# Kernel tuning notes

Hardware: AMD Instinct MI355X
Metric: run time of the kernel (lower is better)

## Reference

```python
import jax, jax.numpy as jnp
import numpy as np

B, H_IMG, W_IMG = 8, 64, 64
C, HEADS, SR, MSG = 128, 4, 4, 4
N0 = H_IMG * W_IMG


def _linear(x, w, b):
    return x @ w.T + b


def _layernorm(x, g, b, eps=1e-5):
    mu = jnp.mean(x, -1, keepdims=True)
    var = jnp.mean(jnp.square(x - mu), -1, keepdims=True)
    return (x - mu) * jax.lax.rsqrt(var + eps) * g + b


def _conv2d(x, w, b, stride, pad, groups=1):
    y = jax.lax.conv_general_dilated(
        x, w, (stride, stride), [(pad, pad), (pad, pad)],
        dimension_numbers=("NCHW", "OIHW", "NCHW"), feature_group_count=groups)
    return y + b[None, :, None, None]


def setup_inputs():
    key = jax.random.key(0)
    ks = jax.random.split(key, 16)
    def nrm(k, shape, std=0.02):
        return jax.random.normal(k, shape, jnp.float32) * std
    z = lambda *s: jnp.zeros(s, jnp.float32)
    return {
        "x": jax.random.normal(ks[0], (B, N0, C), jnp.float32),
        "msg_tokens": jax.random.normal(ks[1], (B, MSG, C), jnp.float32),
        "Wq": nrm(ks[2], (C, C)), "bq": z(C),
        "sr1_w": nrm(ks[3], (C, C, 4, 4), float(np.sqrt(2.0 / (16 * C)))), "sr1_b": z(C),
        "ln1_g": jnp.ones((C,), jnp.float32), "ln1_b": z(C),
        "sr2_w": nrm(ks[4], (C, C, 2, 2), float(np.sqrt(2.0 / (4 * C)))), "sr2_b": z(C),
        "ln2_g": jnp.ones((C,), jnp.float32), "ln2_b": z(C),
        "kv1_w": nrm(ks[5], (C, C)), "kv1_b": z(C),
        "kv2_w": nrm(ks[6], (C, C)), "kv2_b": z(C),
        "lc1_w": nrm(ks[7], (C // 2, 1, 3, 3), float(np.sqrt(2.0 / 9.0))), "lc1_b": z(C // 2),
        "lc2_w": nrm(ks[8], (C // 2, 1, 3, 3), float(np.sqrt(2.0 / 9.0))), "lc2_b": z(C // 2),
        "proj_w": nrm(ks[9], (C, C)), "proj_b": z(C),
        "H": H_IMG, "W": W_IMG,
    }


def reference(x, msg_tokens, Wq, bq, sr1_w, sr1_b, ln1_g, ln1_b,
              sr2_w, sr2_b, ln2_g, ln2_b, kv1_w, kv1_b, kv2_w, kv2_b,
              lc1_w, lc1_b, lc2_w, lc2_b, proj_w, proj_b, H, W):
    Bsz, _, Cc = x.shape
    m = msg_tokens.shape[1]
    h = HEADS
    dh = Cc // h
    scale = dh ** -0.5
    x_q = jnp.concatenate([x, msg_tokens], axis=1)       # [B, N, C]
    N = x_q.shape[1]
    q = _linear(x_q, Wq, bq).reshape(Bsz, N, h, dh).transpose(0, 2, 1, 3)  # [B,h,N,dh]
    x_img = x.transpose(0, 2, 1).reshape(Bsz, Cc, H, W)

    def branch(sr_w, sr_b, ln_g, ln_b, kv_w, kv_b, lc_w, lc_b, q_half, stride):
        Hr, Wr = H // stride, W // stride
        L = Hr * Wr
        # spatial reduction conv -> tokens
        xr = _conv2d(x_img, sr_w, sr_b, stride, 0).reshape(Bsz, Cc, L).transpose(0, 2, 1)
        # message tokens pass through the SR conv via summed weights
        msg_r = jnp.einsum('bnc,oc->bno', msg_tokens, sr_w.sum((-1, -2))) + sr_b
        xk = jax.nn.gelu(_layernorm(jnp.concatenate([xr, msg_r], 1), ln_g, ln_b), approximate=False)
        kv = _linear(xk, kv_w, kv_b).reshape(Bsz, L + m, 2, h // 2, dh).transpose(2, 0, 3, 1, 4)
        k, v = kv[0], kv[1]                               # [B, h/2, L+m, dh]
        attn = jax.nn.softmax(jnp.einsum('bhnd,bhld->bhnl', q_half, k) * scale, axis=-1)
        # fused depthwise conv on the spatial part of V (message tokens bypass)
        v_flat = v.transpose(0, 2, 1, 3).reshape(Bsz, L + m, Cc // 2).transpose(0, 2, 1)  # [B,C/2,L+m]
        lc = _conv2d(v_flat[:, :, :L].reshape(Bsz, Cc // 2, Hr, Wr), lc_w, lc_b, 1, 1,
                     groups=Cc // 2).reshape(Bsz, Cc // 2, L)
        v_add = jnp.concatenate([lc, v_flat[:, :, L:]], axis=2)
        v = v + v_add.reshape(Bsz, h // 2, dh, L + m).transpose(0, 1, 3, 2)
        return jnp.einsum('bhnl,bhld->bhnd', attn, v).transpose(0, 2, 1, 3).reshape(Bsz, N, Cc // 2)

    x1 = branch(sr1_w, sr1_b, ln1_g, ln1_b, kv1_w, kv1_b, lc1_w, lc1_b, q[:, :h // 2], SR)
    x2 = branch(sr2_w, sr2_b, ln2_g, ln2_b, kv2_w, kv2_b, lc2_w, lc2_b, q[:, h // 2:], SR // 2)
    out = _linear(jnp.concatenate([x1, x2], -1), proj_w, proj_b)
    out = x_q + out                                       # identity = x_q, drop_path = Identity
    return out[:, :-m], out[:, -m:]
```

## Files before the change

kernel.cpp:

```cpp
#include <hip/hip_runtime.h>
#include <math.h>

#define BB 8
#define CC 128
#define N0 4096
#define MSGN 4
#define NTOT 4100
#define IMG 64
#define NPAD 4224
#define LMP1 320
#define LMP2 1088

#define OFF_WFQ    0
#define OFF_WFKV1  8192
#define OFF_WFKV2  16384
#define OFF_WFPROJ 24576
#define OFF_WFSR1  32768
#define OFF_WFSR2  163840
#define OFF_QH     196608
#define OFF_XK1    2359296
#define OFF_XK2    2492416
#define OFF_KV1O   3018752
#define OFF_KV2O   3284992
#define OFF_KH1    4337664
#define OFF_VT1    4419584
#define OFF_KH2    4501504
#define OFF_VT2    4780032
#define OFF_XP     5058560

typedef _Float16 half8v __attribute__((ext_vector_type(8)));
typedef _Float16 half4v __attribute__((ext_vector_type(4)));
typedef float f32x4 __attribute__((ext_vector_type(4)));

__device__ __forceinline__ size_t af_idx(int m, int k, int Kc) {
    return ((size_t)((m >> 4) * Kc + (k >> 5)) * 64 + ((k >> 3) & 3) * 16 + (m & 15)) * 8 + (k & 7);
}

__device__ __forceinline__ float exp2_fast(float x) {
#if __has_builtin(__builtin_amdgcn_exp2f)
    return __builtin_amdgcn_exp2f(x);
#else
    return __expf(x * 0.6931471805599453f);
#endif
}

__device__ __forceinline__ void gload16(const _Float16* g, _Float16* l) {
    __builtin_amdgcn_global_load_lds(
        (const __attribute__((address_space(1))) unsigned int*)g,
        (__attribute__((address_space(3))) unsigned int*)l, 16, 0, 0);
}

__global__ void prep_weights(const float* __restrict__ Wq, const float* __restrict__ kv1,
                             const float* __restrict__ kv2, const float* __restrict__ proj,
                             const float* __restrict__ sr1w, const float* __restrict__ sr2w,
                             float* __restrict__ ws, _Float16* __restrict__ Qh) {
    int u = blockIdx.x * blockDim.x + threadIdx.x;
    if (u >= 49152) {
        int idx = u - 49152;
        if (idx >= BB * 4 * (NPAD - NTOT) * 32) return;
        int d = idx & 31;
        int rest = idx >> 5;
        int n = NTOT + rest % (NPAD - NTOT);
        int rest2 = rest / (NPAD - NTOT);
        int hg = rest2 & 3;
        int b = rest2 >> 2;
        Qh[((size_t)(b * 4 + hg) * NPAD + n) * 32 + d] = (_Float16)0.f;
        return;
    }
    int seg, base;
    const float* w = nullptr;
    _Float16* dst;
    if (u < 2048)        { seg = 0; base = u;          w = Wq;   dst = (_Float16*)(ws + OFF_WFQ); }
    else if (u < 4096)   { seg = 0; base = u - 2048;   w = kv1;  dst = (_Float16*)(ws + OFF_WFKV1); }
    else if (u < 6144)   { seg = 0; base = u - 4096;   w = kv2;  dst = (_Float16*)(ws + OFF_WFKV2); }
    else if (u < 8192)   { seg = 0; base = u - 6144;   w = proj; dst = (_Float16*)(ws + OFF_WFPROJ); }
    else if (u < 40960)  { seg = 1; base = u - 8192;   w = sr1w; dst = (_Float16*)(ws + OFF_WFSR1); }
    else                 { seg = 2; base = u - 40960;  w = sr2w; dst = (_Float16*)(ws + OFF_WFSR2); }
    int lane = base & 63;
    int t = (base >> 6) & 7;
    int kc = base >> 9;
    int n = t * 16 + (lane & 15);
    int k0 = kc * 32 + (lane >> 4) * 8;
    half8v val;
    #pragma unroll
    for (int j = 0; j < 8; ++j) {
        int k = k0 + j;
        float v;
        if (seg == 0) v = w[n * 128 + k];
        else if (seg == 1) v = w[(n * 128 + (k & 127)) * 16 + (k >> 7)];
        else v = w[(n * 128 + (k & 127)) * 4 + (k >> 7)];
        val[j] = (_Float16)v;
    }
    *(half8v*)(dst + (size_t)base * 8) = val;
}

template<int S, int WR, int LL, int LM, int KW>
__device__ __forceinline__ void sr_partial(
    int mtile, int kcbase, int lane, const float* __restrict__ x,
    const float* __restrict__ msg, const _Float16* __restrict__ Wf, f32x4 acc[8]) {
    int m15 = lane & 15, quadk = lane >> 4;
    int m = mtile * 16 + m15;
    bool valid = m < BB * LM;
    const float* base = x;
    bool isimg = false;
    if (valid) {
        int b = m / LM, tok = m - b * LM;
        if (tok < LL) {
            int hr = tok / WR, wr = tok - hr * WR;
            base = x + ((size_t)b * N0 + hr * S * IMG + wr * S) * 128;
            isimg = true;
        } else {
            base = msg + ((size_t)b * MSGN + (tok - LL)) * 128;
        }
    }
    const half8v* Bp = (const half8v*)Wf + lane;
    for (int kk = 0; kk < KW; ++kk) {
        int kc = kcbase + kk;
        int k0 = (kc * 4 + quadk) * 8;
        int c = k0 & 127, ij = k0 >> 7;
        half8v a;
        if (valid) {
            int off;
            if (isimg) {
                int ki = ij / S, kj = ij - ki * S;
                off = (ki * IMG + kj) * 128 + c;
            } else off = c;
            const float4* p4 = (const float4*)(base + off);
            float4 f0 = p4[0], f1 = p4[1];
            a[0] = (_Float16)f0.x; a[1] = (_Float16)f0.y; a[2] = (_Float16)f0.z; a[3] = (_Float16)f0.w;
            a[4] = (_Float16)f1.x; a[5] = (_Float16)f1.y; a[6] = (_Float16)f1.z; a[7] = (_Float16)f1.w;
        } else {
            #pragma unroll
            for (int j = 0; j < 8; ++j) a[j] = (_Float16)0.f;
        }
        #pragma unroll
        for (int t = 0; t < 8; ++t)
            acc[t] = __builtin_amdgcn_mfma_f32_16x16x32_f16(a, Bp[(size_t)(kc * 8 + t) * 64], acc[t], 0, 0, 0);
    }
}

__global__ __launch_bounds__(256) void input_gemms(
    const float* __restrict__ x, const float* __restrict__ msg,
    const _Float16* __restrict__ Wf1, const _Float16* __restrict__ Wf2,
    const float* __restrict__ b1, const float* __restrict__ g1, const float* __restrict__ be1,
    const float* __restrict__ b2, const float* __restrict__ g2, const float* __restrict__ be2,
    _Float16* __restrict__ XK1, _Float16* __restrict__ XK2,
    const _Float16* __restrict__ WfQ, const float* __restrict__ bq,
    _Float16* __restrict__ Qh) {
    __shared__ float red[4][2048];
    int tid = threadIdx.x;
    int lane = tid & 63, wave = tid >> 6;
    int bid = blockIdx.x;

    if (bid >= 261) {
        int u = (bid - 261) * 4 + wave;
        int mt = u >> 1, nh = u & 1;
        int m15 = lane & 15, quadk = lane >> 4;
        int m = mt * 16 + m15;
        bool valid = m < BB * NTOT;
        const float* rowp = x;
        if (valid) {
            int b = m / NTOT, n = m - b * NTOT;
            rowp = (n < N0) ? (x + ((size_t)b * N0 + n) * 128)
                            : (msg + ((size_t)b * MSGN + (n - N0)) * 128);
        }
        const half8v* Bp = (const half8v*)WfQ + lane;
        f32x4 acc[4];
        #pragma unroll
        for (int t = 0; t < 4; ++t) acc[t] = (f32x4){0.f, 0.f, 0.f, 0.f};
        #pragma unroll
        for (int kc = 0; kc < 4; ++kc) {
            half8v a;
            if (valid) {
                const float4* p4 = (const float4*)(rowp + (kc * 4 + quadk) * 8);
                float4 f0 = p4[0], f1 = p4[1];
                a[0] = (_Float16)f0.x; a[1] = (_Float16)f0.y; a[2] = (_Float16)f0.z; a[3] = (_Float16)f0.w;
                a[4] = (_Float16)f1.x; a[5] = (_Float16)f1.y; a[6] = (_Float16)f1.z; a[7] = (_Float16)f1.w;
            } else {
                #pragma unroll
                for (int j = 0; j < 8; ++j) a[j] = (_Float16)0.f;
            }
            #pragma unroll
            for (int t = 0; t < 4; ++t)
                acc[t] = __builtin_amdgcn_mfma_f32_16x16x32_f16(a, Bp[(size_t)(kc * 8 + nh * 4 + t) * 64], acc[t], 0, 0, 0);
        }
        int quad = lane >> 4, n15 = lane & 15;
        const float qscale = 0.17677669529663687f * 1.4426950408889634f;
        #pragma unroll
        for (int r = 0; r < 4; ++r) {
            int mm = mt * 16 + quad * 4 + r;
            if (mm >= BB * NTOT) continue;
            int b = mm / NTOT, tok = mm - b * NTOT;
            #pragma unroll
            for (int t = 0; t < 4; ++t) {
                int n = nh * 64 + t * 16 + n15;
                Qh[((size_t)(b * 4 + (n >> 5)) * NPAD + tok) * 32 + (n & 31)] =
                    (_Float16)((acc[t][r] + bq[n]) * qscale);
            }
        }
        return;
    }

    if (bid >= 132) {
        int mtile = (bid - 132) * 4 + wave;
        f32x4 acc[8];
        #pragma unroll
        for (int t = 0; t < 8; ++t) acc[t] = (f32x4){0.f, 0.f, 0.f, 0.f};
        sr_partial<2, 32, 1024, 1028, 16>(mtile, 0, lane, x, msg, Wf2, acc);
        int quad = lane >> 4, n15 = lane & 15;
        float bb[8], gg[8], eb[8];
        #pragma unroll
        for (int j = 0; j < 8; ++j) {
            bb[j] = b2[j * 16 + n15];
            gg[j] = g2[j * 16 + n15];
            eb[j] = be2[j * 16 + n15];
        }
        #pragma unroll
        for (int r = 0; r < 4; ++r) {
            int m = mtile * 16 + quad * 4 + r;
            float s = 0.f;
            #pragma unroll
            for (int j = 0; j < 8; ++j) s += acc[j][r] + bb[j];
            #pragma unroll
            for (int off = 1; off < 16; off <<= 1) s += __shfl_xor(s, off);
            float mu = s * (1.f / 128.f);
            float q = 0.f;
            #pragma unroll
            for (int j = 0; j < 8; ++j) { float d = acc[j][r] + bb[j] - mu; q += d * d; }
            #pragma unroll
            for (int off = 1; off < 16; off <<= 1) q += __shfl_xor(q, off);
            float rs = rsqrtf(q * (1.f / 128.f) + 1e-5f);
            if (m < 8224) {
                #pragma unroll
                for (int j = 0; j < 8; ++j) {
                    float y = (acc[j][r] + bb[j] - mu) * rs * gg[j] + eb[j];
                    y = 0.5f * y * (1.f + erff(y * 0.70710678118654752f));
                    XK2[af_idx(m, j * 16 + n15, 4)] = (_Float16)y;
                }
            }
        }
        return;
    }

    f32x4 acc[8];
    #pragma unroll
    for (int t = 0; t < 8; ++t) acc[t] = (f32x4){0.f, 0.f, 0.f, 0.f};
    int mtile = bid;
    sr_partial<4, 16, 256, 260, 16>(mtile, wave * 16, lane, x, msg, Wf1, acc);
    int quad = lane >> 4, n15 = lane & 15;
    #pragma unroll
    for (int t = 0; t < 8; ++t)
        #pragma unroll
        for (int r = 0; r < 4; ++r)
            red[wave][(quad * 4 + r) * 128 + t * 16 + n15] = acc[t][r];
    __syncthreads();
    for (int e = tid; e < 2048; e += 256)
        red[0][e] = red[0][e] + red[1][e] + red[2][e] + red[3][e];
    __syncthreads();
    int r16 = tid >> 4, l16 = tid & 15;
    int m = mtile * 16 + r16;
    float v[8];
    float s = 0.f;
    #pragma unroll
    for (int j = 0; j < 8; ++j) { v[j] = red[0][r16 * 128 + j * 16 + l16] + b1[j * 16 + l16]; s += v[j]; }
    #pragma unroll
    for (int off = 1; off < 16; off <<= 1) s += __shfl_xor(s, off);
    float mu = s * (1.f / 128.f);
    float q = 0.f;
    #pragma unroll
    for (int j = 0; j < 8; ++j) { v[j] -= mu; q += v[j] * v[j]; }
    #pragma unroll
    for (int off = 1; off < 16; off <<= 1) q += __shfl_xor(q, off);
    float rs = rsqrtf(q * (1.f / 128.f) + 1e-5f);
    if (m < 2080) {
        #pragma unroll
        for (int j = 0; j < 8; ++j) {
            int n = j * 16 + l16;
            float y = v[j] * rs * g1[n] + be1[n];
            y = 0.5f * y * (1.f + erff(y * 0.70710678118654752f));
            XK1[af_idx(m, n, 4)] = (_Float16)y;
        }
    }
}

__global__ __launch_bounds__(256) void kv_gemm(
    const _Float16* __restrict__ XK1, const _Float16* __restrict__ XK2,
    const _Float16* __restrict__ Wf1, const _Float16* __restrict__ Wf2,
    const float* __restrict__ b1, const float* __restrict__ b2,
    float* __restrict__ o1, float* __restrict__ o2) {
    int lane = threadIdx.x & 63, wave = threadIdx.x >> 6;
    int u = blockIdx.x * 4 + wave;
    int t = u >> 1, nh = u & 1;
    int lt;
    const half8v* Ap;
    const half8v* Bp;
    const float* bias;
    float* outp;
    if (t < 130) { lt = t;       Ap = (const half8v*)XK1 + (size_t)lt * 4 * 64 + lane; Bp = (const half8v*)Wf1 + lane; bias = b1; outp = o1; }
    else         { lt = t - 130; Ap = (const half8v*)XK2 + (size_t)lt * 4 * 64 + lane; Bp = (const half8v*)Wf2 + lane; bias = b2; outp = o2; }
    f32x4 acc[4];
    #pragma unroll
    for (int tt = 0; tt < 4; ++tt) acc[tt] = (f32x4){0.f, 0.f, 0.f, 0.f};
    #pragma unroll
    for (int kc = 0; kc < 4; ++kc) {
        half8v a = Ap[(size_t)kc * 64];
        #pragma unroll
        for (int tt = 0; tt < 4; ++tt)
            acc[tt] = __builtin_amdgcn_mfma_f32_16x16x32_f16(a, Bp[(size_t)(kc * 8 + nh * 4 + tt) * 64], acc[tt], 0, 0, 0);
    }
    int quad = lane >> 4, n15 = lane & 15;
    #pragma unroll
    for (int r = 0; r < 4; ++r) {
        int m = lt * 16 + quad * 4 + r;
        #pragma unroll
        for (int tt = 0; tt < 4; ++tt) {
            int n = nh * 64 + tt * 16 + n15;
            outp[(size_t)m * 128 + n] = acc[tt][r] + bias[n];
        }
    }
}

__global__ void pack_kv(const float* __restrict__ kv1o, const float* __restrict__ kv2o,
                        const float* __restrict__ lc1w, const float* __restrict__ lc1b,
                        const float* __restrict__ lc2w, const float* __restrict__ lc2b,
                        _Float16* __restrict__ Kh1, _Float16* __restrict__ Vt1,
                        _Float16* __restrict__ Kh2, _Float16* __restrict__ Vt2) {
    int idx = blockIdx.x * 256 + threadIdx.x;
    const int T1 = BB * LMP1 * 64;
    const float* kv;
    const float* lcw;
    const float* lcb;
    _Float16* Kh;
    _Float16* Vt;
    int Wr, L, Lm, Lmp, li;
    if (idx < T1) { li = idx;      kv = kv1o; lcw = lc1w; lcb = lc1b; Kh = Kh1; Vt = Vt1; Wr = 16; L = 256;  Lm = 260;  Lmp = LMP1; }
    else          { li = idx - T1; kv = kv2o; lcw = lc2w; lcb = lc2b; Kh = Kh2; Vt = Vt2; Wr = 32; L = 1024; Lm = 1028; Lmp = LMP2; }
    int ch = li & 63;
    int rest = li >> 6;
    int n = rest % Lmp;
    int b = rest / Lmp;
    int h2 = ch >> 5, d = ch & 31;
    int Hr = L / Wr;
    float kval = 0.f, vnew = 0.f;
    if (n < Lm) {
        const float* kvb = kv + (size_t)b * Lm * 128;
        kval = kvb[(size_t)n * 128 + ch];
        float v = kvb[(size_t)n * 128 + 64 + ch];
        float add;
        if (n < L) {
            int hr = n / Wr, wr = n - hr * Wr;
            float sum = lcb[ch];
            #pragma unroll
            for (int ki = 0; ki < 3; ++ki)
                #pragma unroll
                for (int kj = 0; kj < 3; ++kj) {
                    int y = hr + ki - 1, xx = wr + kj - 1;
                    if ((unsigned)y < (unsigned)Hr && (unsigned)xx < (unsigned)Wr)
                        sum += lcw[ch * 9 + ki * 3 + kj] * kvb[((size_t)y * Wr + xx) * 128 + 64 + ch];
                }
            add = sum;
        } else {
            add = v;
        }
        vnew = v + add;
    }
    Kh[((size_t)(b * 2 + h2) * Lmp + n) * 32 + d] = (_Float16)kval;
    Vt[(size_t)(b * 2 + h2) * Lmp * 32 + (size_t)(n >> 2) * 128
       + (d & 15) * 8 + ((d >> 4) << 2) + (n & 3)] = (_Float16)vnew;
}

__global__ __launch_bounds__(256, 4) void attn_mfma(
    const _Float16* __restrict__ Qh,
    const _Float16* __restrict__ Kh1, const _Float16* __restrict__ Vt1,
    const _Float16* __restrict__ Kh2, const _Float16* __restrict__ Vt2,
    _Float16* __restrict__ XP) {
    __shared__ _Float16 sK[2][2048];
    __shared__ _Float16 sV[2][2048];
    int tid = threadIdx.x;
    int lane = tid & 63, wave = tid >> 6;
    int b = blockIdx.y;
    int z = blockIdx.z;
    int h2 = z & 1, br = 1 - (z >> 1);
    int tile = blockIdx.x * 4 + wave;
    int n0 = tile * 32;
    int q16 = lane & 15, quad = lane >> 4;
    const f32x4 zf = {0.f, 0.f, 0.f, 0.f};
    int NT = br ? (LMP2 / 64) : (LMP1 / 64);
    int Lmp = br ? LMP2 : LMP1;
    const _Float16* kb = (br ? Kh2 : Kh1) + (size_t)(b * 2 + h2) * Lmp * 32;
    const _Float16* vb = (br ? Vt2 : Vt1) + (size_t)(b * 2 + h2) * Lmp * 32;
    int hg = br * 2 + h2;
    const _Float16* qp = Qh + ((size_t)(b * 4 + hg) * NPAD + n0 + q16) * 32 + quad * 8;
    half8v qf0 = *(const half8v*)qp;
    half8v qf1 = *(const half8v*)(qp + 512);
    f32x4 O00 = zf, O01 = zf, O10 = zf, O11 = zf;
    float la = 0.f, lb = 0.f;

    int ksrc = (wave * 16 + q16) * 32 + quad * 8;
    int vsrc = wave * 512 + lane * 8;

    gload16(kb + ksrc, &sK[0][wave * 512]);
    gload16(vb + vsrc, &sV[0][wave * 512]);
    __syncthreads();

    for (int t = 0; t < NT; ++t) {
        int cur = t & 1;
        if (t + 1 < NT) {
            size_t o = (size_t)(t + 1) * 2048;
            gload16(kb + o + ksrc, &sK[cur ^ 1][wave * 512]);
            gload16(vb + o + vsrc, &sV[cur ^ 1][wave * 512]);
        }
        half8v kf[4], vv[4];
        #pragma unroll
        for (int i = 0; i < 4; ++i)
            kf[i] = *(const half8v*)&sK[cur][i * 512 + lane * 8];
        #pragma unroll
        for (int i = 0; i < 4; ++i)
            vv[i] = *(const half8v*)&sV[cur][i * 512 + quad * 128 + q16 * 8];

        half4v p0[4], p1[4];
        #pragma unroll
        for (int i = 0; i < 4; ++i) {
            f32x4 s0 = __builtin_amdgcn_mfma_f32_16x16x32_f16(kf[i], qf0, zf, 0, 0, 0);
            f32x4 s1 = __builtin_amdgcn_mfma_f32_16x16x32_f16(kf[i], qf1, zf, 0, 0, 0);
            half4v a, c;
            #pragma unroll
            for (int r = 0; r < 4; ++r) {
                float e0 = exp2_fast(s0[r]); la += e0; a[r] = (_Float16)e0;
                float e1 = exp2_fast(s1[r]); lb += e1; c[r] = (_Float16)e1;
            }
            p0[i] = a; p1[i] = c;
        }
        #pragma unroll
        for (int i = 0; i < 4; ++i) {
            half4v v0 = __builtin_shufflevector(vv[i], vv[i], 0, 1, 2, 3);
            half4v v1 = __builtin_shufflevector(vv[i], vv[i], 4, 5, 6, 7);
            O00 = __builtin_amdgcn_mfma_f32_16x16x16f16(p0[i], v0, O00, 0, 0, 0);
            O01 = __builtin_amdgcn_mfma_f32_16x16x16f16(p0[i], v1, O01, 0, 0, 0);
            O10 = __builtin_amdgcn_mfma_f32_16x16x16f16(p1[i], v0, O10, 0, 0, 0);
            O11 = __builtin_amdgcn_mfma_f32_16x16x16f16(p1[i], v1, O11, 0, 0, 0);
        }
        __syncthreads();
    }

    la += __shfl_xor(la, 16); la += __shfl_xor(la, 32);
    lb += __shfl_xor(lb, 16); lb += __shfl_xor(lb, 32);
    la -= 60.0f; lb -= 60.0f;
    float ia = 1.0f / la;
    float ib = 1.0f / lb;

    int kbase = br * 64 + h2 * 32;
    #pragma unroll
    for (int r = 0; r < 4; ++r) {
        int row = quad * 4 + r;
        int src = (lane & 48) | row;
        float fa = __shfl(ia, src);
        float fb = __shfl(ib, src);
        int n = n0 + row;
        if (n < NTOT) {
            int m = b * NTOT + n;
            XP[af_idx(m, kbase + q16, 4)] = (_Float16)(O00[r] * fa);
            XP[af_idx(m, kbase + 16 + q16, 4)] = (_Float16)(O01[r] * fa);
        }
        int n2 = n + 16;
        if (n2 < NTOT) {
            int m = b * NTOT + n2;
            XP[af_idx(m, kbase + q16, 4)] = (_Float16)(O10[r] * fb);
            XP[af_idx(m, kbase + 16 + q16, 4)] = (_Float16)(O11[r] * fb);
        }
    }
}

__global__ __launch_bounds__(256) void proj_gemm(
    const _Float16* __restrict__ XP,
    const _Float16* __restrict__ Wf, const float* __restrict__ bias,
    float* __restrict__ out_f32, const float* __restrict__ x, const float* __restrict__ msg) {
    int lane = threadIdx.x & 63, wave = threadIdx.x >> 6;
    int u = blockIdx.x * 4 + wave;
    int mt = u >> 1, nh = u & 1;
    const half8v* Ap = (const half8v*)XP + (size_t)mt * 4 * 64 + lane;
    const half8v* Bp = (const half8v*)Wf + lane;
    f32x4 acc[4];
    #pragma unroll
    for (int t = 0; t < 4; ++t) acc[t] = (f32x4){0.f, 0.f, 0.f, 0.f};
    #pragma unroll
    for (int kc = 0; kc < 4; ++kc) {
        half8v a = Ap[(size_t)kc * 64];
        #pragma unroll
        for (int t = 0; t < 4; ++t)
            acc[t] = __builtin_amdgcn_mfma_f32_16x16x32_f16(a, Bp[(size_t)(kc * 8 + nh * 4 + t) * 64], acc[t], 0, 0, 0);
    }
    int quad = lane >> 4, n15 = lane & 15;
    #pragma unroll
    for (int r = 0; r < 4; ++r) {
        int m = mt * 16 + quad * 4 + r;
        if (m >= BB * NTOT) continue;
        int b = m / NTOT, tok = m - b * NTOT;
        const float* rp;
        float* dst;
        if (tok < N0) {
            rp = x + ((size_t)b * N0 + tok) * 128;
            dst = out_f32 + ((size_t)b * N0 + tok) * 128;
        } else {
            rp = msg + ((size_t)b * MSGN + (tok - N0)) * 128;
            dst = out_f32 + (size_t)BB * N0 * 128 + ((size_t)b * MSGN + (tok - N0)) * 128;
        }
        #pragma unroll
        for (int t = 0; t < 4; ++t) {
            int n = nh * 64 + t * 16 + n15;
            dst[n] = acc[t][r] + bias[n] + rp[n];
        }
    }
}

extern "C" void kernel_launch(void* const* d_in, const int* in_sizes, int n_in,
                              void* d_out, int out_size, void* d_ws, size_t ws_size,
                              hipStream_t stream) {
    const float* x     = (const float*)d_in[0];
    const float* msg   = (const float*)d_in[1];
    const float* Wq    = (const float*)d_in[2];
    const float* bq    = (const float*)d_in[3];
    const float* sr1w  = (const float*)d_in[4];
    const float* sr1b  = (const float*)d_in[5];
    const float* ln1g  = (const float*)d_in[6];
    const float* ln1b  = (const float*)d_in[7];
    const float* sr2w  = (const float*)d_in[8];
    const float* sr2b  = (const float*)d_in[9];
    const float* ln2g  = (const float*)d_in[10];
    const float* ln2b  = (const float*)d_in[11];
    const float* kv1w  = (const float*)d_in[12];
    const float* kv1b  = (const float*)d_in[13];
    const float* kv2w  = (const float*)d_in[14];
    const float* kv2b  = (const float*)d_in[15];
    const float* lc1w  = (const float*)d_in[16];
    const float* lc1b  = (const float*)d_in[17];
    const float* lc2w  = (const float*)d_in[18];
    const float* lc2b  = (const float*)d_in[19];
    const float* projw = (const float*)d_in[20];
    const float* projb = (const float*)d_in[21];
    float* ws  = (float*)d_ws;
    float* out = (float*)d_out;

    _Float16* WfQ    = (_Float16*)(ws + OFF_WFQ);
    _Float16* WfKV1  = (_Float16*)(ws + OFF_WFKV1);
    _Float16* WfKV2  = (_Float16*)(ws + OFF_WFKV2);
    _Float16* WfPROJ = (_Float16*)(ws + OFF_WFPROJ);
    _Float16* WfSR1  = (_Float16*)(ws + OFF_WFSR1);
    _Float16* WfSR2  = (_Float16*)(ws + OFF_WFSR2);
    _Float16* Qh     = (_Float16*)(ws + OFF_QH);
    _Float16* XP     = (_Float16*)(ws + OFF_XP);
    _Float16* XK1    = (_Float16*)(ws + OFF_XK1);
    _Float16* XK2    = (_Float16*)(ws + OFF_XK2);
    float* kv1o      = ws + OFF_KV1O;
    float* kv2o      = ws + OFF_KV2O;
    _Float16* Kh1    = (_Float16*)(ws + OFF_KH1);
    _Float16* Vt1    = (_Float16*)(ws + OFF_VT1);
    _Float16* Kh2    = (_Float16*)(ws + OFF_KH2);
    _Float16* Vt2    = (_Float16*)(ws + OFF_VT2);

    prep_weights<<<688, 256, 0, stream>>>(Wq, kv1w, kv2w, projw, sr1w, sr2w, ws, Qh);
    input_gemms<<<1286, 256, 0, stream>>>(x, msg, WfSR1, WfSR2,
                                          sr1b, ln1g, ln1b, sr2b, ln2g, ln2b,
                                          XK1, XK2, WfQ, bq, Qh);
    kv_gemm<<<322, 256, 0, stream>>>(XK1, XK2, WfKV1, WfKV2, kv1b, kv2b, kv1o, kv2o);
    pack_kv<<<2816, 256, 0, stream>>>(kv1o, kv2o, lc1w, lc1b, lc2w, lc2b,
                                      Kh1, Vt1, Kh2, Vt2);
    attn_mfma<<<dim3(33, 8, 4), 256, 0, stream>>>(Qh, Kh1, Vt1, Kh2, Vt2, XP);
    proj_gemm<<<1025, 256, 0, stream>>>(XP, WfPROJ, projb, out, x, msg);
}
```

Baseline: 190.9 us.

## Fuse KV GEMM into input_gemms epilogue and compute softmax denominators via MFMA

The KV projection GEMM now runs inside input_gemms, reading the LayerNorm+GELU output from shared memory instead of a global XK buffer. The K half is written directly in the head-packed fp16 layout and only V goes to a smaller fp32 buffer, which removes the separate kv_gemm launch and halves the data pack_kv reads. K padding rows are now zeroed in prep_weights. In attention, the row sums are accumulated by an extra MFMA against a ones vector instead of scalar adds plus shuffles, which adds matrix work but removes VALU and cross-lane reductions.

```diff
diff --git a/kernel.cpp b/kernel.cpp
--- a/kernel.cpp
+++ b/kernel.cpp
@@ -53,11 +53,27 @@
 __global__ void prep_weights(const float* __restrict__ Wq, const float* __restrict__ kv1,
                              const float* __restrict__ kv2, const float* __restrict__ proj,
                              const float* __restrict__ sr1w, const float* __restrict__ sr2w,
-                             float* __restrict__ ws, _Float16* __restrict__ Qh) {
+                             float* __restrict__ ws, _Float16* __restrict__ Qh,
+                             _Float16* __restrict__ Kh1, _Float16* __restrict__ Kh2) {
     int u = blockIdx.x * blockDim.x + threadIdx.x;
+    if (u >= 176128) {
+        int e = u - 176128;
+        int d = e & 31;
+        int rest = e >> 5;
+        if (rest < 960) {
+            int n = 260 + rest % 60;
+            int bh = rest / 60;
+            Kh1[((size_t)bh * LMP1 + n) * 32 + d] = (_Float16)0.f;
+        } else {
+            rest -= 960;
+            int n = 1028 + rest % 60;
+            int bh = rest / 60;
+            Kh2[((size_t)bh * LMP2 + n) * 32 + d] = (_Float16)0.f;
+        }
+        return;
+    }
     if (u >= 49152) {
         int idx = u - 49152;
-        if (idx >= BB * 4 * (NPAD - NTOT) * 32) return;
         int d = idx & 31;
         int rest = idx >> 5;
         int n = NTOT + rest % (NPAD - NTOT);
@@ -144,13 +160,17 @@
     const _Float16* __restrict__ Wf1, const _Float16* __restrict__ Wf2,
     const float* __restrict__ b1, const float* __restrict__ g1, const float* __restrict__ be1,
     const float* __restrict__ b2, const float* __restrict__ g2, const float* __restrict__ be2,
-    _Float16* __restrict__ XK1, _Float16* __restrict__ XK2,
+    const _Float16* __restrict__ WfKV1, const _Float16* __restrict__ WfKV2,
+    const float* __restrict__ kvb1, const float* __restrict__ kvb2,
+    _Float16* __restrict__ Kh1, float* __restrict__ vo1,
+    _Float16* __restrict__ Kh2, float* __restrict__ vo2,
     const _Float16* __restrict__ WfQ, const float* __restrict__ bq,
     _Float16* __restrict__ Qh) {
     __shared__ float red[4][2048];
     int tid = threadIdx.x;
     int lane = tid & 63, wave = tid >> 6;
     int bid = blockIdx.x;
+    const f32x4 zf4 = {0.f, 0.f, 0.f, 0.f};
 
     if (bid >= 261) {
         int u = (bid - 261) * 4 + wave;
@@ -167,7 +187,7 @@
         const half8v* Bp = (const half8v*)WfQ + lane;
         f32x4 acc[4];
         #pragma unroll
-        for (int t = 0; t < 4; ++t) acc[t] = (f32x4){0.f, 0.f, 0.f, 0.f};
+        for (int t = 0; t < 4; ++t) acc[t] = zf4;
         #pragma unroll
         for (int kc = 0; kc < 4; ++kc) {
             half8v a;
@@ -205,7 +225,7 @@
         int mtile = (bid - 132) * 4 + wave;
         f32x4 acc[8];
         #pragma unroll
-        for (int t = 0; t < 8; ++t) acc[t] = (f32x4){0.f, 0.f, 0.f, 0.f};
+        for (int t = 0; t < 8; ++t) acc[t] = zf4;
         sr_partial<2, 32, 1024, 1028, 16>(mtile, 0, lane, x, msg, Wf2, acc);
         int quad = lane >> 4, n15 = lane & 15;
         float bb[8], gg[8], eb[8];
@@ -215,9 +235,9 @@
             gg[j] = g2[j * 16 + n15];
             eb[j] = be2[j * 16 + n15];
         }
+        _Float16* XKw = (_Float16*)(&red[0][0]) + wave * 2176;
         #pragma unroll
         for (int r = 0; r < 4; ++r) {
-            int m = mtile * 16 + quad * 4 + r;
             float s = 0.f;
             #pragma unroll
             for (int j = 0; j < 8; ++j) s += acc[j][r] + bb[j];
@@ -230,12 +250,38 @@
             #pragma unroll
             for (int off = 1; off < 16; off <<= 1) q += __shfl_xor(q, off);
             float rs = rsqrtf(q * (1.f / 128.f) + 1e-5f);
-            if (m < 8224) {
-                #pragma unroll
-                for (int j = 0; j < 8; ++j) {
-                    float y = (acc[j][r] + bb[j] - mu) * rs * gg[j] + eb[j];
-                    y = 0.5f * y * (1.f + erff(y * 0.70710678118654752f));
-                    XK2[af_idx(m, j * 16 + n15, 4)] = (_Float16)y;
+            #pragma unroll
+            for (int j = 0; j < 8; ++j) {
+                float y = (acc[j][r] + bb[j] - mu) * rs * gg[j] + eb[j];
+                y = 0.5f * y * (1.f + erff(y * 0.70710678118654752f));
+                XKw[(quad * 4 + r) * 136 + j * 16 + n15] = (_Float16)y;
+            }
+        }
+        __syncthreads();
+        const half8v* Bp = (const half8v*)WfKV2 + lane;
+        f32x4 ka[8];
+        #pragma unroll
+        for (int tt = 0; tt < 8; ++tt) ka[tt] = zf4;
+        #pragma unroll
+        for (int kc = 0; kc < 4; ++kc) {
+            half8v a = *(const half8v*)&XKw[(lane & 15) * 136 + kc * 32 + (lane >> 4) * 8];
+            #pragma unroll
+            for (int tt = 0; tt < 8; ++tt)
+                ka[tt] = __builtin_amdgcn_mfma_f32_16x16x32_f16(a, Bp[(size_t)(kc * 8 + tt) * 64], ka[tt], 0, 0, 0);
+        }
+        #pragma unroll
+        for (int r = 0; r < 4; ++r) {
+            int m = mtile * 16 + quad * 4 + r;
+            if (m >= 8224) continue;
+            int b = m / 1028, tok = m - b * 1028;
+            #pragma unroll
+            for (int tt = 0; tt < 8; ++tt) {
+                int n = tt * 16 + n15;
+                float val = ka[tt][r] + kvb2[n];
+                if (tt < 4) {
+                    Kh2[((size_t)(b * 2 + (n >> 5)) * LMP2 + tok) * 32 + (n & 31)] = (_Float16)val;
+                } else {
+                    vo2[((size_t)b * 1028 + tok) * 64 + (n - 64)] = val;
                 }
             }
         }
@@ -244,7 +290,7 @@
 
     f32x4 acc[8];
     #pragma unroll
-    for (int t = 0; t < 8; ++t) acc[t] = (f32x4){0.f, 0.f, 0.f, 0.f};
+    for (int t = 0; t < 8; ++t) acc[t] = zf4;
     int mtile = bid;
     sr_partial<4, 16, 256, 260, 16>(mtile, wave * 16, lane, x, msg, Wf1, acc);
     int quad = lane >> 4, n15 = lane & 15;
@@ -272,80 +318,70 @@
     #pragma unroll
     for (int off = 1; off < 16; off <<= 1) q += __shfl_xor(q, off);
     float rs = rsqrtf(q * (1.f / 128.f) + 1e-5f);
+    _Float16* XKs = (_Float16*)(&red[1][0]);
     if (m < 2080) {
         #pragma unroll
         for (int j = 0; j < 8; ++j) {
-            int n = j * 16 + l16;
-            float y = v[j] * rs * g1[n] + be1[n];
+            float y = v[j] * rs * g1[j * 16 + l16] + be1[j * 16 + l16];
             y = 0.5f * y * (1.f + erff(y * 0.70710678118654752f));
-            XK1[af_idx(m, n, 4)] = (_Float16)y;
-        }
-    }
-}
-
-__global__ __launch_bounds__(256) void kv_gemm(
-    const _Float16* __restrict__ XK1, const _Float16* __restrict__ XK2,
-    const _Float16* __restrict__ Wf1, const _Float16* __restrict__ Wf2,
-    const float* __restrict__ b1, const float* __restrict__ b2,
-    float* __restrict__ o1, float* __restrict__ o2) {
-    int lane = threadIdx.x & 63, wave = threadIdx.x >> 6;
-    int u = blockIdx.x * 4 + wave;
-    int t = u >> 1, nh = u & 1;
-    int lt;
-    const half8v* Ap;
-    const half8v* Bp;
-    const float* bias;
-    float* outp;
-    if (t < 130) { lt = t;       Ap = (const half8v*)XK1 + (size_t)lt * 4 * 64 + lane; Bp = (const half8v*)Wf1 + lane; bias = b1; outp = o1; }
-    else         { lt = t - 130; Ap = (const half8v*)XK2 + (size_t)lt * 4 * 64 + lane; Bp = (const half8v*)Wf2 + lane; bias = b2; outp = o2; }
-    f32x4 acc[4];
-    #pragma unroll
-    for (int tt = 0; tt < 4; ++tt) acc[tt] = (f32x4){0.f, 0.f, 0.f, 0.f};
-    #pragma unroll
-    for (int kc = 0; kc < 4; ++kc) {
-        half8v a = Ap[(size_t)kc * 64];
-        #pragma unroll
-        for (int tt = 0; tt < 4; ++tt)
-            acc[tt] = __builtin_amdgcn_mfma_f32_16x16x32_f16(a, Bp[(size_t)(kc * 8 + nh * 4 + tt) * 64], acc[tt], 0, 0, 0);
-    }
-    int quad = lane >> 4, n15 = lane & 15;
-    #pragma unroll
-    for (int r = 0; r < 4; ++r) {
-        int m = lt * 16 + quad * 4 + r;
-        #pragma unroll
-        for (int tt = 0; tt < 4; ++tt) {
-            int n = nh * 64 + tt * 16 + n15;
-            outp[(size_t)m * 128 + n] = acc[tt][r] + bias[n];
-        }
-    }
-}
-
-__global__ void pack_kv(const float* __restrict__ kv1o, const float* __restrict__ kv2o,
+            XKs[r16 * 136 + j * 16 + l16] = (_Float16)y;
+        }
+    }
+    __syncthreads();
+    {
+        const half8v* Bp = (const half8v*)WfKV1 + lane;
+        int t0 = wave * 2;
+        f32x4 ka[2];
+        ka[0] = zf4; ka[1] = zf4;
+        #pragma unroll
+        for (int kc = 0; kc < 4; ++kc) {
+            half8v a = *(const half8v*)&XKs[(lane & 15) * 136 + kc * 32 + (lane >> 4) * 8];
+            #pragma unroll
+            for (int tt = 0; tt < 2; ++tt)
+                ka[tt] = __builtin_amdgcn_mfma_f32_16x16x32_f16(a, Bp[(size_t)(kc * 8 + t0 + tt) * 64], ka[tt], 0, 0, 0);
+        }
+        #pragma unroll
+        for (int r = 0; r < 4; ++r) {
+            int mm = mtile * 16 + quad * 4 + r;
+            if (mm >= 2080) continue;
+            int b = mm / 260, tok = mm - b * 260;
+            #pragma unroll
+            for (int tt = 0; tt < 2; ++tt) {
+                int n = (t0 + tt) * 16 + n15;
+                float val = ka[tt][r] + kvb1[n];
+                if (n < 64) {
+                    Kh1[((size_t)(b * 2 + (n >> 5)) * LMP1 + tok) * 32 + (n & 31)] = (_Float16)val;
+                } else {
+                    vo1[((size_t)b * 260 + tok) * 64 + (n - 64)] = val;
+                }
+            }
+        }
+    }
+}
+
+__global__ void pack_kv(const float* __restrict__ vo1, const float* __restrict__ vo2,
                         const float* __restrict__ lc1w, const float* __restrict__ lc1b,
                         const float* __restrict__ lc2w, const float* __restrict__ lc2b,
-                        _Float16* __restrict__ Kh1, _Float16* __restrict__ Vt1,
-                        _Float16* __restrict__ Kh2, _Float16* __restrict__ Vt2) {
+                        _Float16* __restrict__ Vt1, _Float16* __restrict__ Vt2) {
     int idx = blockIdx.x * 256 + threadIdx.x;
     const int T1 = BB * LMP1 * 64;
-    const float* kv;
+    const float* vo;
     const float* lcw;
     const float* lcb;
-    _Float16* Kh;
     _Float16* Vt;
     int Wr, L, Lm, Lmp, li;
-    if (idx < T1) { li = idx;      kv = kv1o; lcw = lc1w; lcb = lc1b; Kh = Kh1; Vt = Vt1; Wr = 16; L = 256;  Lm = 260;  Lmp = LMP1; }
-    else          { li = idx - T1; kv = kv2o; lcw = lc2w; lcb = lc2b; Kh = Kh2; Vt = Vt2; Wr = 32; L = 1024; Lm = 1028; Lmp = LMP2; }
+    if (idx < T1) { li = idx;      vo = vo1; lcw = lc1w; lcb = lc1b; Vt = Vt1; Wr = 16; L = 256;  Lm = 260;  Lmp = LMP1; }
+    else          { li = idx - T1; vo = vo2; lcw = lc2w; lcb = lc2b; Vt = Vt2; Wr = 32; L = 1024; Lm = 1028; Lmp = LMP2; }
     int ch = li & 63;
     int rest = li >> 6;
     int n = rest % Lmp;
     int b = rest / Lmp;
     int h2 = ch >> 5, d = ch & 31;
     int Hr = L / Wr;
-    float kval = 0.f, vnew = 0.f;
+    float vnew = 0.f;
     if (n < Lm) {
-        const float* kvb = kv + (size_t)b * Lm * 128;
-        kval = kvb[(size_t)n * 128 + ch];
-        float v = kvb[(size_t)n * 128 + 64 + ch];
+        const float* vb2 = vo + (size_t)b * Lm * 64;
+        float v = vb2[(size_t)n * 64 + ch];
         float add;
         if (n < L) {
             int hr = n / Wr, wr = n - hr * Wr;
@@ -356,7 +392,7 @@
                 for (int kj = 0; kj < 3; ++kj) {
                     int y = hr + ki - 1, xx = wr + kj - 1;
                     if ((unsigned)y < (unsigned)Hr && (unsigned)xx < (unsigned)Wr)
-                        sum += lcw[ch * 9 + ki * 3 + kj] * kvb[((size_t)y * Wr + xx) * 128 + 64 + ch];
+                        sum += lcw[ch * 9 + ki * 3 + kj] * vb2[((size_t)y * Wr + xx) * 64 + ch];
                 }
             add = sum;
         } else {
@@ -364,7 +400,6 @@
         }
         vnew = v + add;
     }
-    Kh[((size_t)(b * 2 + h2) * Lmp + n) * 32 + d] = (_Float16)kval;
     Vt[(size_t)(b * 2 + h2) * Lmp * 32 + (size_t)(n >> 2) * 128
        + (d & 15) * 8 + ((d >> 4) << 2) + (n & 3)] = (_Float16)vnew;
 }
@@ -394,7 +429,10 @@
     half8v qf0 = *(const half8v*)qp;
     half8v qf1 = *(const half8v*)(qp + 512);
     f32x4 O00 = zf, O01 = zf, O10 = zf, O11 = zf;
-    float la = 0.f, lb = 0.f;
+    f32x4 La = zf, Lb = zf;
+    half4v ones4;
+    #pragma unroll
+    for (int r = 0; r < 4; ++r) ones4[r] = (_Float16)1.f;
 
     int ksrc = (wave * 16 + q16) * 32 + quad * 8;
     int vsrc = wave * 512 + lane * 8;
@@ -426,8 +464,8 @@
             half4v a, c;
             #pragma unroll
             for (int r = 0; r < 4; ++r) {
-                float e0 = exp2_fast(s0[r]); la += e0; a[r] = (_Float16)e0;
-                float e1 = exp2_fast(s1[r]); lb += e1; c[r] = (_Float16)e1;
+                a[r] = (_Float16)exp2_fast(s0[r]);
+                c[r] = (_Float16)exp2_fast(s1[r]);
             }
             p0[i] = a; p1[i] = c;
         }
@@ -437,26 +475,20 @@
             half4v v1 = __builtin_shufflevector(vv[i], vv[i], 4, 5, 6, 7);
             O00 = __builtin_amdgcn_mfma_f32_16x16x16f16(p0[i], v0, O00, 0, 0, 0);
             O01 = __builtin_amdgcn_mfma_f32_16x16x16f16(p0[i], v1, O01, 0, 0, 0);
+            La  = __builtin_amdgcn_mfma_f32_16x16x16f16(p0[i], ones4, La, 0, 0, 0);
             O10 = __builtin_amdgcn_mfma_f32_16x16x16f16(p1[i], v0, O10, 0, 0, 0);
             O11 = __builtin_amdgcn_mfma_f32_16x16x16f16(p1[i], v1, O11, 0, 0, 0);
+            Lb  = __builtin_amdgcn_mfma_f32_16x16x16f16(p1[i], ones4, Lb, 0, 0, 0);
         }
         __syncthreads();
     }
 
-    la += __shfl_xor(la, 16); la += __shfl_xor(la, 32);
-    lb += __shfl_xor(lb, 16); lb += __shfl_xor(lb, 32);
-    la -= 60.0f; lb -= 60.0f;
-    float ia = 1.0f / la;
-    float ib = 1.0f / lb;
-
     int kbase = br * 64 + h2 * 32;
     #pragma unroll
     for (int r = 0; r < 4; ++r) {
-        int row = quad * 4 + r;
-        int src = (lane & 48) | row;
-        float fa = __shfl(ia, src);
-        float fb = __shfl(ib, src);
-        int n = n0 + row;
+        float fa = 1.0f / (La[r] - 60.0f);
+        float fb = 1.0f / (Lb[r] - 60.0f);
+        int n = n0 + quad * 4 + r;
         if (n < NTOT) {
             int m = b * NTOT + n;
             XP[af_idx(m, kbase + q16, 4)] = (_Float16)(O00[r] * fa);
@@ -549,22 +581,20 @@
     _Float16* WfSR2  = (_Float16*)(ws + OFF_WFSR2);
     _Float16* Qh     = (_Float16*)(ws + OFF_QH);
     _Float16* XP     = (_Float16*)(ws + OFF_XP);
-    _Float16* XK1    = (_Float16*)(ws + OFF_XK1);
-    _Float16* XK2    = (_Float16*)(ws + OFF_XK2);
-    float* kv1o      = ws + OFF_KV1O;
-    float* kv2o      = ws + OFF_KV2O;
+    float* vo1       = ws + OFF_KV1O;
+    float* vo2       = ws + OFF_KV2O;
     _Float16* Kh1    = (_Float16*)(ws + OFF_KH1);
     _Float16* Vt1    = (_Float16*)(ws + OFF_VT1);
     _Float16* Kh2    = (_Float16*)(ws + OFF_KH2);
     _Float16* Vt2    = (_Float16*)(ws + OFF_VT2);
 
-    prep_weights<<<688, 256, 0, stream>>>(Wq, kv1w, kv2w, projw, sr1w, sr2w, ws, Qh);
+    prep_weights<<<928, 256, 0, stream>>>(Wq, kv1w, kv2w, projw, sr1w, sr2w, ws, Qh, Kh1, Kh2);
     input_gemms<<<1286, 256, 0, stream>>>(x, msg, WfSR1, WfSR2,
                                           sr1b, ln1g, ln1b, sr2b, ln2g, ln2b,
-                                          XK1, XK2, WfQ, bq, Qh);
-    kv_gemm<<<322, 256, 0, stream>>>(XK1, XK2, WfKV1, WfKV2, kv1b, kv2b, kv1o, kv2o);
-    pack_kv<<<2816, 256, 0, stream>>>(kv1o, kv2o, lc1w, lc1b, lc2w, lc2b,
-                                      Kh1, Vt1, Kh2, Vt2);
+                                          WfKV1, WfKV2, kv1b, kv2b,
+                                          Kh1, vo1, Kh2, vo2,
+                                          WfQ, bq, Qh);
+    pack_kv<<<2816, 256, 0, stream>>>(vo1, vo2, lc1w, lc1b, lc2w, lc2b, Vt1, Vt2);
     attn_mfma<<<dim3(33, 8, 4), 256, 0, stream>>>(Qh, Kh1, Vt1, Kh2, Vt2, XP);
     proj_gemm<<<1025, 256, 0, stream>>>(XP, WfPROJ, projb, out, x, msg);
 }
```

Result: faster. 186.5 us (-2.3%).
